# Kernel tuning notes

Hardware: AMD Instinct MI355X
Metric: run time of the kernel (lower is better)

## Reference

```python
import jax, jax.numpy as jnp
import numpy as np

EPS = float(np.finfo(np.float32).eps)


def fake_quant_w(w):
    # per-output-channel symmetric int8 fake quant; w: (out, in)
    w_d = jax.lax.stop_gradient(w)
    max_abs = jnp.max(jnp.abs(w_d), axis=1, keepdims=True)
    scale = jnp.maximum(max_abs / 127.0, EPS)
    w_q = jnp.clip(jnp.round(w_d / scale), -127, 127)
    return w_q * scale


def woq_linear(x, w, b):
    return x @ fake_quant_w(w).T + b


def setup_inputs() -> dict:
    key = jax.random.key(0)
    ks = jax.random.split(key, 9)
    dim = 1024
    B, S = 2, 2048
    def wmat(k):
        return jax.random.normal(k, (dim, dim), dtype=jnp.float32) * (1.0 / np.sqrt(dim))
    def bvec(k):
        return jax.random.normal(k, (dim,), dtype=jnp.float32) * 0.01
    return {
        "x": jax.random.normal(ks[0], (B, S, dim), dtype=jnp.float32),
        "wq": wmat(ks[1]), "bq": bvec(ks[2]),
        "wk": wmat(ks[3]), "bk": bvec(ks[4]),
        "wv": wmat(ks[5]), "bv": bvec(ks[6]),
        "wp": wmat(ks[7]), "bp": bvec(ks[8]),
    }


def reference(x, wq, bq, wk, bk, wv, bv, wp, bp):
    B, S, C = x.shape
    H = 16
    D = C // H
    scale = D ** -0.5
    # QKV projections with fake-quantized weights -> (B, H, S, D)
    q = woq_linear(x, wq, bq).reshape(B, S, H, D).transpose(0, 2, 1, 3)
    k = woq_linear(x, wk, bk).reshape(B, S, H, D).transpose(0, 2, 1, 3)
    v = woq_linear(x, wv, bv).reshape(B, S, H, D).transpose(0, 2, 1, 3)
    attn = jnp.einsum("bhsd,bhtd->bhst", q, k) * scale  # (B,H,S,S)
    attn = jax.nn.softmax(attn, axis=-1)
    out = jnp.einsum("bhst,bhtd->bhsd", attn, v)
    out = out.transpose(0, 2, 1, 3).reshape(B, S, C)
    return woq_linear(out, wp, bp)
```

## Files before the change

kernel.cpp:

```cpp
#include <hip/hip_runtime.h>
#include <stdint.h>

typedef short bf16x8 __attribute__((ext_vector_type(8)));
typedef float f32x4 __attribute__((ext_vector_type(4)));
typedef uint16_t u16;
typedef uint32_t u32;
typedef u16 u16x4 __attribute__((ext_vector_type(4)));

#define EPSF 1.1920929e-07f

static __device__ __forceinline__ u16 f2bf(float f) {
  union { float f; uint32_t u; } v; v.f = f;
  return (u16)((v.u + 0x7FFFu + ((v.u >> 16) & 1u)) >> 16);
}
static __device__ __forceinline__ float bf2f(u16 h) {
  union { uint32_t u; float f; } v; v.u = ((uint32_t)h) << 16;
  return v.f;
}
static __device__ __forceinline__ float exp2_fast(float x) {
  return __builtin_amdgcn_exp2f(x);
}
static __device__ __forceinline__ u32 cvt_pk_bf16(float lo, float hi) {
  u32 r;
  asm("v_cvt_pk_bf16_f32 %0, %1, %2" : "=v"(r) : "v"(lo), "v"(hi));
  return r;
}
static __device__ __forceinline__ void gload_lds16(const void* g, void* l) {
  __builtin_amdgcn_global_load_lds(
      (const __attribute__((address_space(1))) void*)g,
      (__attribute__((address_space(3))) void*)l, 16, 0, 0);
}
template <int N>
static __device__ __forceinline__ void vmwait() {
  asm volatile("s_waitcnt vmcnt(%0)" ::"i"(N) : "memory");
}

__global__ __launch_bounds__(256) void prep_kernel(
    const float* __restrict__ wq, const float* __restrict__ wk,
    const float* __restrict__ wv, const float* __restrict__ wp,
    const float* __restrict__ x,
    u16* __restrict__ wout, float* __restrict__ scales, u16* __restrict__ xb) {
  const int t = threadIdx.x;
  if (blockIdx.x < 4096) {
    const int row = blockIdx.x & 1023;
    const int mat = blockIdx.x >> 10;
    const float* W = (mat == 0) ? wq : (mat == 1) ? wk : (mat == 2) ? wv : wp;
    const float4 v = ((const float4*)(W + (size_t)row * 1024))[t];
    float m = fmaxf(fmaxf(fabsf(v.x), fabsf(v.y)), fmaxf(fabsf(v.z), fabsf(v.w)));
#pragma unroll
    for (int off = 1; off < 64; off <<= 1) m = fmaxf(m, __shfl_xor(m, off));
    __shared__ float red[4];
    if ((t & 63) == 0) red[t >> 6] = m;
    __syncthreads();
    m = fmaxf(fmaxf(red[0], red[1]), fmaxf(red[2], red[3]));
    const float scale = fmaxf(m / 127.0f, EPSF);
    float q0 = fminf(fmaxf(rintf(v.x / scale), -127.f), 127.f);
    float q1 = fminf(fmaxf(rintf(v.y / scale), -127.f), 127.f);
    float q2 = fminf(fmaxf(rintf(v.z / scale), -127.f), 127.f);
    float q3 = fminf(fmaxf(rintf(v.w / scale), -127.f), 127.f);
    u16x4 o; o.x = f2bf(q0); o.y = f2bf(q1); o.z = f2bf(q2); o.w = f2bf(q3);
    *(u16x4*)(wout + ((size_t)(mat * 1024 + row)) * 1024 + t * 4) = o;
    if (t == 0) scales[mat * 1024 + row] = scale;
  } else {
    const int i = (blockIdx.x - 4096) * 256 + t;
    const float4 v = ((const float4*)x)[i];
    u16x4 hv;
    hv.x = f2bf(v.x); hv.y = f2bf(v.y); hv.z = f2bf(v.z); hv.w = f2bf(v.w);
    *(u16x4*)(xb + (size_t)i * 4) = hv;
  }
}

template <int MODE, int MR, int NR, int NT, int KT, int LDA>
__global__ __launch_bounds__(512) void gemm_kernel(
    const u16* __restrict__ A, const u16* __restrict__ Bw,
    const float* __restrict__ scales, const float* __restrict__ b0,
    const float* __restrict__ b1, const float* __restrict__ b2,
    u16* __restrict__ qkv, float* __restrict__ outp) {
  constexpr int BM = 2 * MR * 16;
  constexpr int BN = 4 * NR * 16;
  constexpr int OPS = BM / 64 + BN / 64;
  __shared__ u16 As[2][BM * 64];
  __shared__ u16 Bs[2][BN * 64];
  const int tid = threadIdx.x;
  const int w = tid >> 6, l = tid & 63;
  const int per = gridDim.x >> 3;
  const int L = (blockIdx.x & 7) * per + (blockIdx.x >> 3);
  const int tile_n = (L % NT) * BN;
  const int tile_m = (L / NT) * BM;
  const int wm = w >> 2, wn = w & 3;
  const int l15 = l & 15, l4 = l >> 4;
  const int sw = l15 & 7;

  f32x4 acc[MR][NR];
  const f32x4 vzero = {0.f, 0.f, 0.f, 0.f};
#pragma unroll
  for (int m = 0; m < MR; ++m)
#pragma unroll
    for (int n = 0; n < NR; ++n) acc[m][n] = vzero;

  const int r8 = tid >> 3;
  const int g = tid & 7;
  const int gs = g ^ (r8 & 7);
  auto STAGE = [&](int slot, int j) {
    const int kb = j * 64;
    const int kbB = kb & 1023;
#pragma unroll
    for (int i = 0; i < BM / 64; ++i)
      gload_lds16(A + (size_t)(tile_m + i * 64 + r8) * LDA + kb + gs * 8,
                  &As[slot][(i * 64 + r8) * 64 + g * 8]);
#pragma unroll
    for (int i = 0; i < BN / 64; ++i)
      gload_lds16(Bw + (size_t)(tile_n + i * 64 + r8) * 1024 + kbB + gs * 8,
                  &Bs[slot][(i * 64 + r8) * 64 + g * 8]);
  };

  STAGE(0, 0);
  STAGE(1, 1);
  vmwait<OPS>();
  __builtin_amdgcn_s_barrier();

  for (int j = 0; j < KT; ++j) {
    const int cur = j & 1;
#pragma unroll
    for (int ks = 0; ks < 2; ++ks) {
      bf16x8 af[MR], bfv[NR];
      const int sg8 = ((ks * 4 + l4) ^ sw) * 8;
#pragma unroll
      for (int m = 0; m < MR; ++m)
        af[m] = *(const bf16x8*)(&As[cur][(wm * (MR * 16) + m * 16 + l15) * 64 + sg8]);
#pragma unroll
      for (int n = 0; n < NR; ++n)
        bfv[n] = *(const bf16x8*)(&Bs[cur][(wn * (NR * 16) + n * 16 + l15) * 64 + sg8]);
      __builtin_amdgcn_s_setprio(1);
#pragma unroll
      for (int m = 0; m < MR; ++m)
#pragma unroll
        for (int n = 0; n < NR; ++n)
          acc[m][n] = __builtin_amdgcn_mfma_f32_16x16x32_bf16(af[m], bfv[n], acc[m][n], 0, 0, 0);
      __builtin_amdgcn_s_setprio(0);
    }
    __builtin_amdgcn_s_barrier();
    if (j + 2 < KT) {
      STAGE(cur, j + 2);
      vmwait<OPS>();
    } else {
      vmwait<0>();
    }
    __builtin_amdgcn_s_barrier();
  }

#pragma unroll
  for (int m = 0; m < MR; ++m) {
#pragma unroll
    for (int n = 0; n < NR; ++n) {
      const int col = tile_n + wn * (NR * 16) + n * 16 + l15;
      const float sc = scales[col];
      if constexpr (MODE == 0) {
        const int mat = col >> 10, oo = col & 1023;
        const float* bias = (mat == 0) ? b0 : (mat == 1) ? b1 : b2;
        const float bb = bias[oo];
        const int hh = oo >> 6, dd = oo & 63;
        if (mat == 2) {
          const int rowm0 = tile_m + wm * (MR * 16) + m * 16 + l4 * 4;
          const int b = rowm0 >> 11, s = rowm0 & 2047;
          u16x4 pk;
#pragma unroll
          for (int jj = 0; jj < 4; ++jj) pk[jj] = f2bf(acc[m][n][jj] * sc + bb);
          *(u16x4*)(qkv + (size_t)2 * 4194304 +
                    ((size_t)(b * 16 + hh) * 64 + dd) * 2048 + s) = pk;
        } else {
#pragma unroll
          for (int jj = 0; jj < 4; ++jj) {
            const int rowm = tile_m + wm * (MR * 16) + m * 16 + l4 * 4 + jj;
            const int b = rowm >> 11, s = rowm & 2047;
            float y = acc[m][n][jj] * sc + bb;
            if (mat == 0) y *= 0.18033688011112042f;
            qkv[(size_t)mat * 4194304 + ((size_t)(b * 16 + hh) * 2048 + s) * 64 + dd] = f2bf(y);
          }
        }
      } else {
        const float bb = b0[col];
#pragma unroll
        for (int jj = 0; jj < 4; ++jj) {
          const int rowm = tile_m + wm * (MR * 16) + m * 16 + l4 * 4 + jj;
          outp[(size_t)rowm * 1024 + col] = acc[m][n][jj] * sc + bb;
        }
      }
    }
  }
}

__global__ __launch_bounds__(512) void attn_kernel(
    const u16* __restrict__ qg, const u16* __restrict__ kg,
    const u16* __restrict__ vtg, u16* __restrict__ po) {
  __shared__ u16 Kt[2][128 * 64];
  __shared__ u16 Vt[2][64 * 128];
  __shared__ u16 Pl[8 * 16 * 64];
  const int tid = threadIdx.x;
  const int w = tid >> 6, l = tid & 63;
  const int Lb = (blockIdx.x & 7) * 64 + (blockIdx.x >> 3);
  const int bh = Lb >> 4;
  const int qt = Lb & 15;
  const u16* qp = qg + (size_t)bh * 131072;
  const u16* kp = kg + (size_t)bh * 131072;
  const u16* vp = vtg + (size_t)bh * 131072;
  const int qrow0 = qt * 128 + w * 16;
  const int l15 = l & 15, l4 = l >> 4;
  const int sw = l15 & 7;

  auto STAGE = [&](int slot, int kt) {
#pragma unroll
    for (int i = 0; i < 2; ++i) {
      const int rk = i * 64 + (tid >> 3);
      gload_lds16(kp + (size_t)(kt + rk) * 64 + (((tid & 7) ^ (rk & 7)) << 3),
                  &Kt[slot][i * 4096 + tid * 8]);
    }
#pragma unroll
    for (int i = 0; i < 2; ++i) {
      const int rv = i * 32 + (tid >> 4);
      gload_lds16(vp + (size_t)rv * 2048 + kt + (((tid & 15) ^ (rv & 7)) << 3),
                  &Vt[slot][i * 4096 + tid * 8]);
    }
  };

  bf16x8 qf[2];
#pragma unroll
  for (int dk = 0; dk < 2; ++dk)
    qf[dk] = *(const bf16x8*)(qp + (size_t)(qrow0 + l15) * 64 + dk * 32 + l4 * 8);

  const f32x4 vzero = {0.f, 0.f, 0.f, 0.f};
  f32x4 O[4];
#pragma unroll
  for (int di = 0; di < 4; ++di) O[di] = vzero;
  float lrun = 0.f;

  STAGE(0, 0);
  STAGE(1, 128);
  vmwait<4>();
  __builtin_amdgcn_s_barrier();

  for (int j = 0; j < 16; ++j) {
    const int cur = j & 1;

    f32x4 sfr[8];
#pragma unroll
    for (int ki = 0; ki < 8; ++ki) sfr[ki] = vzero;
#pragma unroll
    for (int dk = 0; dk < 2; ++dk) {
      bf16x8 kf[8];
#pragma unroll
      for (int ki = 0; ki < 8; ++ki)
        kf[ki] = *(const bf16x8*)(&Kt[cur][(ki * 16 + l15) * 64 + (((dk * 4 + l4) ^ sw) << 3)]);
      __builtin_amdgcn_s_setprio(1);
#pragma unroll
      for (int ki = 0; ki < 8; ++ki)
        sfr[ki] = __builtin_amdgcn_mfma_f32_16x16x32_bf16(kf[ki], qf[dk], sfr[ki], 0, 0, 0);
      __builtin_amdgcn_s_setprio(0);
    }

#pragma unroll
    for (int half = 0; half < 2; ++half) {
      float rs = 0.f;
      u32 pw[8];
#pragma unroll
      for (int ki = 0; ki < 4; ++ki) {
        const f32x4 s4 = sfr[half * 4 + ki];
        const float p0 = exp2_fast(s4[0]);
        const float p1 = exp2_fast(s4[1]);
        const float p2 = exp2_fast(s4[2]);
        const float p3 = exp2_fast(s4[3]);
        rs += (p0 + p1) + (p2 + p3);
        pw[ki * 2 + 0] = cvt_pk_bf16(p0, p1);
        pw[ki * 2 + 1] = cvt_pk_bf16(p2, p3);
      }
      lrun += rs;

      u32* pb = (u32*)Pl + w * 512 + l15 * 32;
#pragma unroll
      for (int ki = 0; ki < 4; ++ki) {
#pragma unroll
        for (int h = 0; h < 2; ++h) {
          const int W = ki * 8 + l4 * 2 + h;
          pb[(((W >> 2) ^ sw) << 2) + (W & 3)] = pw[ki * 2 + h];
        }
      }

#pragma unroll
      for (int kkl = 0; kkl < 2; ++kkl) {
        const bf16x8 pf =
            *(const bf16x8*)(Pl + w * 1024 + l15 * 64 + (((kkl * 4 + l4) ^ sw) << 3));
        bf16x8 vf[4];
#pragma unroll
        for (int di = 0; di < 4; ++di)
          vf[di] = *(const bf16x8*)(&Vt[cur][(di * 16 + l15) * 128 +
                                             (((half * 8 + kkl * 4 + l4) ^ sw) << 3)]);
        __builtin_amdgcn_s_setprio(1);
#pragma unroll
        for (int di = 0; di < 4; ++di)
          O[di] = __builtin_amdgcn_mfma_f32_16x16x32_bf16(pf, vf[di], O[di], 0, 0, 0);
        __builtin_amdgcn_s_setprio(0);
      }
    }

    __builtin_amdgcn_s_barrier();
    if (j + 2 < 16) {
      STAGE(cur, (j + 2) * 128);
      vmwait<4>();
    } else {
      vmwait<0>();
    }
    __builtin_amdgcn_s_barrier();
  }

  lrun += __shfl_xor(lrun, 16);
  lrun += __shfl_xor(lrun, 32);
  const int b = bh >> 4, hh = bh & 15;
  float lq[4];
#pragma unroll
  for (int jj = 0; jj < 4; ++jj)
    lq[jj] = __builtin_amdgcn_rcpf(__shfl(lrun, l4 * 4 + jj));
#pragma unroll
  for (int di = 0; di < 4; ++di)
#pragma unroll
    for (int jj = 0; jj < 4; ++jj) {
      const float oval = O[di][jj] * lq[jj];
      const int srw = qrow0 + l4 * 4 + jj;
      const int c = hh * 64 + di * 16 + l15;
      const u16 hi = f2bf(oval);
      const u16 lo = f2bf(oval - bf2f(hi));
      const size_t base = ((size_t)(b * 2048 + srw)) * 2048;
      po[base + c] = hi;
      po[base + 1024 + c] = lo;
    }
}

extern "C" void kernel_launch(void* const* d_in, const int* in_sizes, int n_in,
                              void* d_out, int out_size, void* d_ws, size_t ws_size,
                              hipStream_t stream) {
  (void)in_sizes; (void)n_in; (void)out_size; (void)ws_size;
  const float* x  = (const float*)d_in[0];
  const float* wq = (const float*)d_in[1];
  const float* bq = (const float*)d_in[2];
  const float* wk = (const float*)d_in[3];
  const float* bk = (const float*)d_in[4];
  const float* wv = (const float*)d_in[5];
  const float* bv = (const float*)d_in[6];
  const float* wp = (const float*)d_in[7];
  const float* bp = (const float*)d_in[8];

  char* ws = (char*)d_ws;
  u16*   wquant = (u16*)ws;
  float* scales = (float*)(ws + 8388608);
  u16*   xb     = (u16*)(ws + 8404992);
  u16*   po     = xb;
  u16*   qkv    = (u16*)(ws + 25182208);

  prep_kernel<<<dim3(8192), dim3(256), 0, stream>>>(
      wq, wk, wv, wp, x, wquant, scales, xb);
  gemm_kernel<0, 4, 3, 16, 16, 1024><<<dim3(512), dim3(512), 0, stream>>>(
      xb, wquant, scales, bq, bk, bv, qkv, nullptr);
  attn_kernel<<<dim3(512), dim3(512), 0, stream>>>(
      qkv, qkv + 4194304, qkv + 8388608, po);
  gemm_kernel<1, 2, 2, 8, 32, 2048><<<dim3(512), dim3(512), 0, stream>>>(
      po, wquant + 3145728, scales + 3072, bp, nullptr, nullptr, nullptr, (float*)d_out);
}
```

Measured before the change: 118.2 us.

## Keep P in registers, drop split-bf16 attention output, halve projection K

```diff
diff --git a/kernel.cpp b/kernel.cpp
--- a/kernel.cpp
+++ b/kernel.cpp
@@ -6,6 +6,8 @@
 typedef uint16_t u16;
 typedef uint32_t u32;
 typedef u16 u16x4 __attribute__((ext_vector_type(4)));
+typedef u32 u32x2 __attribute__((ext_vector_type(2)));
+typedef u32 u32x4 __attribute__((ext_vector_type(4)));
 
 #define EPSF 1.1920929e-07f
 
@@ -190,12 +192,11 @@
   }
 }
 
-__global__ __launch_bounds__(512) void attn_kernel(
+__global__ __launch_bounds__(512, 4) void attn_kernel(
     const u16* __restrict__ qg, const u16* __restrict__ kg,
     const u16* __restrict__ vtg, u16* __restrict__ po) {
   __shared__ u16 Kt[2][128 * 64];
   __shared__ u16 Vt[2][64 * 128];
-  __shared__ u16 Pl[8 * 16 * 64];
   const int tid = threadIdx.x;
   const int w = tid >> 6, l = tid & 63;
   const int Lb = (blockIdx.x & 7) * 64 + (blockIdx.x >> 3);
@@ -208,7 +209,7 @@
   const int l15 = l & 15, l4 = l >> 4;
   const int sw = l15 & 7;
 
-  auto STAGE = [&](int slot, int kt) {
+  auto STAGE = [&](const int slot, const int kt) {
 #pragma unroll
     for (int i = 0; i < 2; ++i) {
       const int rk = i * 64 + (tid >> 3);
@@ -223,10 +224,10 @@
     }
   };
 
-  bf16x8 qf[2];
+  bf16x8 qfr[2];
 #pragma unroll
   for (int dk = 0; dk < 2; ++dk)
-    qf[dk] = *(const bf16x8*)(qp + (size_t)(qrow0 + l15) * 64 + dk * 32 + l4 * 8);
+    qfr[dk] = *(const bf16x8*)(qp + (size_t)(qrow0 + l15) * 64 + dk * 32 + l4 * 8);
 
   const f32x4 vzero = {0.f, 0.f, 0.f, 0.f};
   f32x4 O[4];
@@ -234,14 +235,7 @@
   for (int di = 0; di < 4; ++di) O[di] = vzero;
   float lrun = 0.f;
 
-  STAGE(0, 0);
-  STAGE(1, 128);
-  vmwait<4>();
-  __builtin_amdgcn_s_barrier();
-
-  for (int j = 0; j < 16; ++j) {
-    const int cur = j & 1;
-
+  auto DO_ITER = [&](const int slot, const int j) {
     f32x4 sfr[8];
 #pragma unroll
     for (int ki = 0; ki < 8; ++ki) sfr[ki] = vzero;
@@ -250,18 +244,18 @@
       bf16x8 kf[8];
 #pragma unroll
       for (int ki = 0; ki < 8; ++ki)
-        kf[ki] = *(const bf16x8*)(&Kt[cur][(ki * 16 + l15) * 64 + (((dk * 4 + l4) ^ sw) << 3)]);
+        kf[ki] = *(const bf16x8*)(&Kt[slot][(ki * 16 + l15) * 64 + (((dk * 4 + l4) ^ sw) << 3)]);
       __builtin_amdgcn_s_setprio(1);
 #pragma unroll
       for (int ki = 0; ki < 8; ++ki)
-        sfr[ki] = __builtin_amdgcn_mfma_f32_16x16x32_bf16(kf[ki], qf[dk], sfr[ki], 0, 0, 0);
+        sfr[ki] = __builtin_amdgcn_mfma_f32_16x16x32_bf16(kf[ki], qfr[dk], sfr[ki], 0, 0, 0);
       __builtin_amdgcn_s_setprio(0);
     }
 
 #pragma unroll
     for (int half = 0; half < 2; ++half) {
+      u32 pw[8];
       float rs = 0.f;
-      u32 pw[8];
 #pragma unroll
       for (int ki = 0; ki < 4; ++ki) {
         const f32x4 s4 = sfr[half * 4 + ki];
@@ -275,46 +269,54 @@
       }
       lrun += rs;
 
-      u32* pb = (u32*)Pl + w * 512 + l15 * 32;
-#pragma unroll
-      for (int ki = 0; ki < 4; ++ki) {
-#pragma unroll
-        for (int h = 0; h < 2; ++h) {
-          const int W = ki * 8 + l4 * 2 + h;
-          pb[(((W >> 2) ^ sw) << 2) + (W & 3)] = pw[ki * 2 + h];
+#pragma unroll
+      for (int kkl = 0; kkl < 2; ++kkl) {
+        const int c = half * 2 + kkl;
+        const u32x4 t0 = {pw[kkl * 4 + 0], pw[kkl * 4 + 1],
+                          pw[kkl * 4 + 2], pw[kkl * 4 + 3]};
+        const bf16x8 pf0 = __builtin_bit_cast(bf16x8, t0);
+        const int o0 = (((c * 4 + (l4 >> 1)) ^ sw) << 3) + (l4 & 1) * 4;
+        const int o1 = (((c * 4 + 2 + (l4 >> 1)) ^ sw) << 3) + (l4 & 1) * 4;
+        bf16x8 vf[4];
+#pragma unroll
+        for (int di = 0; di < 4; ++di) {
+          const u16* vrow = &Vt[slot][(di * 16 + l15) * 128];
+          const u32x2 lo = *(const u32x2*)(vrow + o0);
+          const u32x2 hi = *(const u32x2*)(vrow + o1);
+          const u32x4 q = {lo.x, lo.y, hi.x, hi.y};
+          vf[di] = __builtin_bit_cast(bf16x8, q);
         }
-      }
-
-#pragma unroll
-      for (int kkl = 0; kkl < 2; ++kkl) {
-        const bf16x8 pf =
-            *(const bf16x8*)(Pl + w * 1024 + l15 * 64 + (((kkl * 4 + l4) ^ sw) << 3));
-        bf16x8 vf[4];
+        __builtin_amdgcn_s_setprio(1);
 #pragma unroll
         for (int di = 0; di < 4; ++di)
-          vf[di] = *(const bf16x8*)(&Vt[cur][(di * 16 + l15) * 128 +
-                                             (((half * 8 + kkl * 4 + l4) ^ sw) << 3)]);
-        __builtin_amdgcn_s_setprio(1);
-#pragma unroll
-        for (int di = 0; di < 4; ++di)
-          O[di] = __builtin_amdgcn_mfma_f32_16x16x32_bf16(pf, vf[di], O[di], 0, 0, 0);
+          O[di] = __builtin_amdgcn_mfma_f32_16x16x32_bf16(pf0, vf[di], O[di], 0, 0, 0);
         __builtin_amdgcn_s_setprio(0);
       }
     }
 
     __builtin_amdgcn_s_barrier();
     if (j + 2 < 16) {
-      STAGE(cur, (j + 2) * 128);
+      STAGE(slot, (j + 2) * 128);
       vmwait<4>();
     } else {
       vmwait<0>();
     }
     __builtin_amdgcn_s_barrier();
+  };
+
+  STAGE(0, 0);
+  STAGE(1, 128);
+  vmwait<4>();
+  __builtin_amdgcn_s_barrier();
+
+  for (int jp = 0; jp < 8; ++jp) {
+    DO_ITER(0, jp * 2);
+    DO_ITER(1, jp * 2 + 1);
   }
 
+  const int b = bh >> 4, hh = bh & 15;
   lrun += __shfl_xor(lrun, 16);
   lrun += __shfl_xor(lrun, 32);
-  const int b = bh >> 4, hh = bh & 15;
   float lq[4];
 #pragma unroll
   for (int jj = 0; jj < 4; ++jj)
@@ -326,11 +328,7 @@
       const float oval = O[di][jj] * lq[jj];
       const int srw = qrow0 + l4 * 4 + jj;
       const int c = hh * 64 + di * 16 + l15;
-      const u16 hi = f2bf(oval);
-      const u16 lo = f2bf(oval - bf2f(hi));
-      const size_t base = ((size_t)(b * 2048 + srw)) * 2048;
-      po[base + c] = hi;
-      po[base + 1024 + c] = lo;
+      po[((size_t)(b * 2048 + srw)) * 1024 + c] = f2bf(oval);
     }
 }
 
@@ -361,6 +359,6 @@
       xb, wquant, scales, bq, bk, bv, qkv, nullptr);
   attn_kernel<<<dim3(512), dim3(512), 0, stream>>>(
       qkv, qkv + 4194304, qkv + 8388608, po);
-  gemm_kernel<1, 2, 2, 8, 32, 2048><<<dim3(512), dim3(512), 0, stream>>>(
+  gemm_kernel<1, 2, 2, 8, 16, 1024><<<dim3(512), dim3(512), 0, stream>>>(
       po, wquant + 3145728, scales + 3072, bp, nullptr, nullptr, nullptr, (float*)d_out);
 }
```

New measurement: 117.2 us. Within noise of the previous version (-0.9%).
